# Kernel optimization log

Measured on AMD Instinct MI355X. Metric: run time of the kernel, lower is better.

The kernel has to match this reference:

```python
import jax, jax.numpy as jnp
import numpy as np

N_NODES = 100000
N_EDGES = 3200000
F_DIM = 128
UNITS = 128
K_HOPS = 3


def setup_inputs() -> dict:
    key = jax.random.key(0)
    k1, k2, k3, k4, k5 = jax.random.split(key, 5)
    edge_rows = jax.random.randint(k1, (N_EDGES,), 0, N_NODES, dtype=jnp.int32)
    edge_cols = jax.random.randint(k2, (N_EDGES,), 0, N_NODES, dtype=jnp.int32)
    # positive edge weights (e.g. normalized adjacency values)
    edge_vals = jax.random.uniform(k3, (N_EDGES,), dtype=jnp.float32) / 32.0
    x = jax.random.normal(k4, (N_NODES, F_DIM), dtype=jnp.float32)
    H = jax.random.normal(k5, (K_HOPS, F_DIM, UNITS), dtype=jnp.float32) * 0.05
    return {"edge_rows": edge_rows, "edge_cols": edge_cols,
            "edge_vals": edge_vals, "x": x, "H": H}


def reference(edge_rows, edge_cols, edge_vals, x, H):
    # spmm(h) = A @ h, with A given as an edge list (rows, cols, vals).
    def spmm(h):
        # gather source features, scale by edge weight, scatter-add to dest rows
        return jax.ops.segment_sum(edge_vals[:, None] * h[edge_cols],
                                   edge_rows, num_segments=N_NODES)

    # output = sum_{k=0}^{K-1} S_k @ (X @ H_k), S_0 = I, S_k = A^k
    out = x @ H[0]  # k = 0: identity propagation
    for k in range(1, K_HOPS):
        t = x @ H[k]           # [N, units] skinny GEMM
        for _ in range(k):     # apply A k times -> A^k @ t
            t = spmm(t)
        out = out + t
    return out  # activation is identity in defaults
```

## Files before the change

kernel.cpp:

```cpp
#include <hip/hip_runtime.h>

#define NN 100000
#define NE 3200000
#define FD 128
#define NBUK 782
#define NSEG (NBUK * 8)
#define NBIN 1024
#define CHUNK (NE / NBIN)
#define MAXB 5120

typedef __attribute__((ext_vector_type(8))) short short8;
typedef __attribute__((ext_vector_type(4))) float f32x4;

__device__ inline unsigned int f2bf_bits(float x) {
    unsigned int u = __float_as_uint(x);
    return (u + 0x7fffu + ((u >> 16) & 1u)) >> 16;
}
__device__ inline float bf_lo(unsigned int u) { return __uint_as_float(u << 16); }
__device__ inline float bf_hi(unsigned int u) { return __uint_as_float(u & 0xffff0000u); }

__global__ __launch_bounds__(256)
void cvt_x(const float* __restrict__ X, unsigned short* __restrict__ Xbf) {
    const int total = NN * FD / 4;
    const int stride = gridDim.x * blockDim.x;
    for (int i = blockIdx.x * blockDim.x + threadIdx.x; i < total; i += stride) {
        float4 v = reinterpret_cast<const float4*>(X)[i];
        uint2 o = make_uint2(f2bf_bits(v.x) | (f2bf_bits(v.y) << 16),
                             f2bf_bits(v.z) | (f2bf_bits(v.w) << 16));
        reinterpret_cast<uint2*>(Xbf)[i] = o;
    }
}

__global__ __launch_bounds__(256)
void cvt_h(const float* __restrict__ H, unsigned short* __restrict__ HbfT) {
    int i = blockIdx.x * 256 + threadIdx.x;
    if (i < 3 * FD * FD) {
        int k   = i >> 14;
        int rem = i & 16383;
        int kk  = rem >> 7;
        int col = rem & 127;
        HbfT[k * (FD * FD) + col * FD + kk] = (unsigned short)f2bf_bits(H[i]);
    }
}

__global__ __launch_bounds__(256, 4)
void gemm3_mfma(const unsigned short* __restrict__ Xbf,
                const unsigned short* __restrict__ HbfT,
                float* __restrict__ OUT,
                unsigned short* __restrict__ Vbf,
                unsigned short* __restrict__ T2bf) {
    __shared__ __align__(16) unsigned short Xs[128 * 128];
    const int tid  = threadIdx.x;
    const int row0 = blockIdx.x * 128;

    #pragma unroll
    for (int it = 0; it < 8; ++it) {
        int c    = it * 256 + tid;
        int r    = c >> 4;
        int col8 = (c & 15) * 8;
        int gr   = row0 + r;
        uint4 v = make_uint4(0u, 0u, 0u, 0u);
        if (gr < NN)
            v = *reinterpret_cast<const uint4*>(Xbf + (size_t)gr * FD + col8);
        int byte = r * 256 + col8 * 2;
        byte ^= (r & 7) << 4;
        *reinterpret_cast<uint4*>(reinterpret_cast<char*>(Xs) + byte) = v;
    }
    __syncthreads();

    const int lane = tid & 63;
    const int w    = tid >> 6;
    const int l15  = lane & 15;
    const int g4   = lane >> 4;

    int abyte[2];
    #pragma unroll
    for (int m = 0; m < 2; ++m) {
        int arow = 32 * w + 16 * m + l15;
        abyte[m] = arow * 256 + g4 * 16;
    }
    const int swz0 = (l15 & 7) << 4;

    #pragma unroll
    for (int h = 0; h < 3; ++h) {
        f32x4 acc[2][8];
        #pragma unroll
        for (int m = 0; m < 2; ++m)
            #pragma unroll
            for (int n = 0; n < 8; ++n) acc[m][n] = (f32x4)(0.f);

        const unsigned short* Hb = HbfT + h * (FD * FD) + l15 * FD + g4 * 8;

        #pragma unroll
        for (int ks = 0; ks < 4; ++ks) {
            short8 a0 = *reinterpret_cast<const short8*>(
                reinterpret_cast<const char*>(Xs) + ((abyte[0] + ks * 64) ^ swz0));
            short8 a1 = *reinterpret_cast<const short8*>(
                reinterpret_cast<const char*>(Xs) + ((abyte[1] + ks * 64) ^ swz0));
            #pragma unroll
            for (int n = 0; n < 8; ++n) {
                short8 b = *reinterpret_cast<const short8*>(Hb + n * (16 * FD) + ks * 32);
                acc[0][n] = __builtin_amdgcn_mfma_f32_16x16x32_bf16(a0, b, acc[0][n], 0, 0, 0);
                acc[1][n] = __builtin_amdgcn_mfma_f32_16x16x32_bf16(a1, b, acc[1][n], 0, 0, 0);
            }
        }

        #pragma unroll
        for (int m = 0; m < 2; ++m) {
            #pragma unroll
            for (int r = 0; r < 4; ++r) {
                int gr = row0 + 32 * w + 16 * m + g4 * 4 + r;
                if (gr < NN) {
                    if (h == 0) {
                        float* dst = OUT + (size_t)gr * FD + l15;
                        #pragma unroll
                        for (int n = 0; n < 8; ++n) dst[16 * n] = acc[m][n][r];
                    } else {
                        unsigned short* dst = (h == 1 ? Vbf : T2bf) + (size_t)gr * FD + l15;
                        #pragma unroll
                        for (int n = 0; n < 8; ++n)
                            dst[16 * n] = (unsigned short)f2bf_bits(acc[m][n][r]);
                    }
                }
            }
        }
    }
}

__global__ __launch_bounds__(256)
void zero_counts(int* __restrict__ counts) {
    int i = blockIdx.x * 256 + threadIdx.x;
    if (i < NSEG) counts[i] = 0;
}

__global__ __launch_bounds__(256)
void bucket_hist(const int* __restrict__ rows, int* __restrict__ counts) {
    __shared__ int lh[NBUK];
    for (int i = threadIdx.x; i < NBUK; i += 256) lh[i] = 0;
    __syncthreads();
    const int beg = blockIdx.x * CHUNK, end = beg + CHUNK;
    for (int e = beg + threadIdx.x; e < end; e += 256)
        atomicAdd(&lh[rows[e] >> 7], 1);
    __syncthreads();
    const int g = blockIdx.x & 7;
    for (int b = threadIdx.x; b < NBUK; b += 256)
        if (lh[b]) atomicAdd(&counts[b * 8 + g], lh[b]);
}

__global__ __launch_bounds__(1024)
void scan_segs(const int* __restrict__ counts, int* __restrict__ cursor,
               int* __restrict__ bucket_ptr) {
    __shared__ int s[1024];
    const int tid = threadIdx.x;
    const int per = (NSEG + 1023) / 1024;
    const int base = tid * per;
    int sum = 0;
    for (int i = 0; i < per; ++i) {
        int idx = base + i;
        if (idx < NSEG) sum += counts[idx];
    }
    s[tid] = sum;
    __syncthreads();
    for (int off = 1; off < 1024; off <<= 1) {
        int t = (tid >= off) ? s[tid - off] : 0;
        __syncthreads();
        s[tid] += t;
        __syncthreads();
    }
    int run = s[tid] - sum;
    for (int i = 0; i < per; ++i) {
        int idx = base + i;
        if (idx < NSEG) {
            cursor[idx] = run;
            if ((idx & 7) == 0) bucket_ptr[idx >> 3] = run;
            run += counts[idx];
        }
    }
    if (tid == 1023) bucket_ptr[NBUK] = NE;
}

__global__ __launch_bounds__(256)
void bin_scatter(const int* __restrict__ rows, const int* __restrict__ cols,
                 const float* __restrict__ vals, int* __restrict__ cursor,
                 uint2* __restrict__ recs) {
    const int beg = blockIdx.x * CHUNK, end = beg + CHUNK;
    const int g = blockIdx.x & 7;
    for (int e = beg + threadIdx.x; e < end; e += 256) {
        int r = rows[e];
        int b = r >> 7;
        int pos = atomicAdd(&cursor[b * 8 + g], 1);
        recs[pos] = make_uint2(((unsigned)(r & 127) << 17) | (unsigned)cols[e],
                               __float_as_uint(vals[e]));
    }
}

__global__ __launch_bounds__(256)
void bucket_csr(uint2* __restrict__ recs, const int* __restrict__ bucket_ptr,
                int* __restrict__ row_ptr) {
    __shared__ uint2 stage[MAXB];
    __shared__ int lh[128];
    __shared__ int lsc[128];
    const int b = blockIdx.x, tid = threadIdx.x;
    const int beg = bucket_ptr[b], end = bucket_ptr[b + 1];
    const int n = end - beg;

    if (tid < 128) lh[tid] = 0;
    __syncthreads();
    for (int i = tid; i < n; i += 256) {
        uint2 r = recs[beg + i];
        stage[i] = r;
        atomicAdd(&lh[r.x >> 17], 1);
    }
    __syncthreads();
    int v = (tid < 128) ? lh[tid] : 0;
    if (tid < 128) lsc[tid] = v;
    __syncthreads();
    for (int off = 1; off < 128; off <<= 1) {
        int t = 0;
        if (tid < 128 && tid >= off) t = lsc[tid - off];
        __syncthreads();
        if (tid < 128) lsc[tid] += t;
        __syncthreads();
    }
    if (tid < 128) {
        int excl = lsc[tid] - v;
        int gr = b * 128 + tid;
        if (gr <= NN) row_ptr[gr] = beg + excl;
        lh[tid] = excl;
    }
    __syncthreads();
    for (int i = tid; i < n; i += 256) {
        uint2 r = stage[i];
        int pos = atomicAdd(&lh[r.x >> 17], 1);
        recs[beg + pos] = r;
    }
}

#define SPMM_BODY(STORE)                                                       \
    const int lane = threadIdx.x & 63;                                         \
    const int row  = (blockIdx.x * blockDim.x + threadIdx.x) >> 6;             \
    if (row >= NN) return;                                                     \
    const int sub = lane >> 5;                     \
    const int fq  = lane & 31;                 \
    const int beg = row_ptr[row], end = row_ptr[row + 1];                      \
    float4 acc = make_float4(0.f, 0.f, 0.f, 0.f);                              \
    int e = beg + sub;                                                         \
    for (; e + 14 < end; e += 16) {                                            \
        uint2 p[8];                                                            \
        uint2 g[8];                                                            \
        _Pragma("unroll")                                                      \
        for (int u = 0; u < 8; ++u) p[u] = recs[e + 2 * u];                    \
        _Pragma("unroll")                                                      \
        for (int u = 0; u < 8; ++u)                                            \
            g[u] = *reinterpret_cast<const uint2*>(                            \
                src + (size_t)(p[u].x & 0x1FFFF) * FD + fq * 4);               \
        _Pragma("unroll")                                                      \
        for (int u = 0; u < 8; ++u) {                                          \
            float v = __uint_as_float(p[u].y);                                 \
            acc.x += v * bf_lo(g[u].x); acc.y += v * bf_hi(g[u].x);            \
            acc.z += v * bf_lo(g[u].y); acc.w += v * bf_hi(g[u].y);            \
        }                                                                      \
    }                                                                          \
    for (; e < end; e += 2) {                                                  \
        uint2 p = recs[e];                                                     \
        uint2 g = *reinterpret_cast<const uint2*>(                             \
            src + (size_t)(p.x & 0x1FFFF) * FD + fq * 4);                      \
        float v = __uint_as_float(p.y);                                        \
        acc.x += v * bf_lo(g.x); acc.y += v * bf_hi(g.x);                      \
        acc.z += v * bf_lo(g.y); acc.w += v * bf_hi(g.y);                      \
    }                                                                          \
    acc.x += __shfl_xor(acc.x, 32, 64);                                        \
    acc.y += __shfl_xor(acc.y, 32, 64);                                        \
    acc.z += __shfl_xor(acc.z, 32, 64);                                        \
    acc.w += __shfl_xor(acc.w, 32, 64);                                        \
    if (sub == 0) { STORE }

__global__ __launch_bounds__(256)
void spmm_bf_bf(const int* __restrict__ row_ptr, const uint2* __restrict__ recs,
                const unsigned short* __restrict__ src,
                unsigned short* __restrict__ initdst) {
    SPMM_BODY({
        uint2 iv = *reinterpret_cast<const uint2*>(initdst + (size_t)row * FD + fq * 4);
        acc.x += bf_lo(iv.x); acc.y += bf_hi(iv.x);
        acc.z += bf_lo(iv.y); acc.w += bf_hi(iv.y);
        unsigned int w0 = f2bf_bits(acc.x) | (f2bf_bits(acc.y) << 16);
        unsigned int w1 = f2bf_bits(acc.z) | (f2bf_bits(acc.w) << 16);
        *reinterpret_cast<uint2*>(initdst + (size_t)row * FD + fq * 4) = make_uint2(w0, w1);
    })
}

__global__ __launch_bounds__(256)
void spmm_bf_f32(const int* __restrict__ row_ptr, const uint2* __restrict__ recs,
                 const unsigned short* __restrict__ src, float* __restrict__ dst) {
    SPMM_BODY({
        float4 iv = *reinterpret_cast<const float4*>(dst + (size_t)row * FD + fq * 4);
        acc.x += iv.x; acc.y += iv.y; acc.z += iv.z; acc.w += iv.w;
        *reinterpret_cast<float4*>(dst + (size_t)row * FD + fq * 4) = acc;
    })
}

extern "C" void kernel_launch(void* const* d_in, const int* in_sizes, int n_in,
                              void* d_out, int out_size, void* d_ws, size_t ws_size,
                              hipStream_t stream) {
    const int*   edge_rows = (const int*)d_in[0];
    const int*   edge_cols = (const int*)d_in[1];
    const float* edge_vals = (const float*)d_in[2];
    const float* x         = (const float*)d_in[3];
    const float* H         = (const float*)d_in[4];
    float*       out       = (float*)d_out;

    const size_t feat = (size_t)NN * FD;
    unsigned short* Xbf  = (unsigned short*)d_ws;
    unsigned short* T2bf = Xbf + feat;
    unsigned short* Vbf  = T2bf + feat;
    unsigned short* HbfT = Vbf + feat;
    uint2*          recs = (uint2*)(HbfT + 3 * FD * FD);
    int* counts     = (int*)(recs + NE);
    int* cursor     = counts + NSEG;
    int* row_ptr    = cursor + NSEG;
    int* bucket_ptr = row_ptr + NN + 1;

    cvt_x<<<2048, 256, 0, stream>>>(x, Xbf);
    cvt_h<<<(3 * FD * FD + 255) / 256, 256, 0, stream>>>(H, HbfT);

    gemm3_mfma<<<(NN + 127) / 128, 256, 0, stream>>>(Xbf, HbfT, out, Vbf, T2bf);

    zero_counts<<<(NSEG + 255) / 256, 256, 0, stream>>>(counts);
    bucket_hist<<<NBIN, 256, 0, stream>>>(edge_rows, counts);
    scan_segs<<<1, 1024, 0, stream>>>(counts, cursor, bucket_ptr);
    bin_scatter<<<NBIN, 256, 0, stream>>>(edge_rows, edge_cols, edge_vals,
                                          cursor, recs);
    bucket_csr<<<NBUK, 256, 0, stream>>>(recs, bucket_ptr, row_ptr);

    const int spmm_blocks = (NN * 64 + 255) / 256;
    spmm_bf_bf <<<spmm_blocks, 256, 0, stream>>>(row_ptr, recs, T2bf, Vbf);
    spmm_bf_f32<<<spmm_blocks, 256, 0, stream>>>(row_ptr, recs, Vbf, out);
}
```

Measured before the change: 651.5 us.

## Fuse X bf16 conversion into GEMM and restructure CSR build into partition sort

The GEMM now reads fp32 X and converts to bf16 while staging into LDS, removing the separate cvt_x pass and its round-trip buffer. The CSR construction switches from 782 buckets of 128 rows with 8 sub-segments to 391 partitions of 256 rows. Per-block local histograms reserve contiguous ranges with one global atomic per partition, so the per-edge global atomics become LDS atomics. A row_sort pass then writes into a second record buffer instead of staging in shared memory. This adds an extra 25.6 MB workspace buffer and re-reads rows in the scatter kernel in exchange for fewer global atomics.

```diff
diff --git a/kernel.cpp b/kernel.cpp
--- a/kernel.cpp
+++ b/kernel.cpp
@@ -3,11 +3,10 @@
 #define NN 100000
 #define NE 3200000
 #define FD 128
-#define NBUK 782
-#define NSEG (NBUK * 8)
-#define NBIN 1024
-#define CHUNK (NE / NBIN)
-#define MAXB 5120
+#define PROWS 256
+#define NPART 391
+#define PBIN 512
+#define PCHUNK (NE / PBIN)
 
 typedef __attribute__((ext_vector_type(8))) short short8;
 typedef __attribute__((ext_vector_type(4))) float f32x4;
@@ -18,18 +17,6 @@
 }
 __device__ inline float bf_lo(unsigned int u) { return __uint_as_float(u << 16); }
 __device__ inline float bf_hi(unsigned int u) { return __uint_as_float(u & 0xffff0000u); }
-
-__global__ __launch_bounds__(256)
-void cvt_x(const float* __restrict__ X, unsigned short* __restrict__ Xbf) {
-    const int total = NN * FD / 4;
-    const int stride = gridDim.x * blockDim.x;
-    for (int i = blockIdx.x * blockDim.x + threadIdx.x; i < total; i += stride) {
-        float4 v = reinterpret_cast<const float4*>(X)[i];
-        uint2 o = make_uint2(f2bf_bits(v.x) | (f2bf_bits(v.y) << 16),
-                             f2bf_bits(v.z) | (f2bf_bits(v.w) << 16));
-        reinterpret_cast<uint2*>(Xbf)[i] = o;
-    }
-}
 
 __global__ __launch_bounds__(256)
 void cvt_h(const float* __restrict__ H, unsigned short* __restrict__ HbfT) {
@@ -44,7 +31,7 @@
 }
 
 __global__ __launch_bounds__(256, 4)
-void gemm3_mfma(const unsigned short* __restrict__ Xbf,
+void gemm3_mfma(const float* __restrict__ X,
                 const unsigned short* __restrict__ HbfT,
                 float* __restrict__ OUT,
                 unsigned short* __restrict__ Vbf,
@@ -60,8 +47,14 @@
         int col8 = (c & 15) * 8;
         int gr   = row0 + r;
         uint4 v = make_uint4(0u, 0u, 0u, 0u);
-        if (gr < NN)
-            v = *reinterpret_cast<const uint4*>(Xbf + (size_t)gr * FD + col8);
+        if (gr < NN) {
+            float4 a = *reinterpret_cast<const float4*>(X + (size_t)gr * FD + col8);
+            float4 b = *reinterpret_cast<const float4*>(X + (size_t)gr * FD + col8 + 4);
+            v.x = f2bf_bits(a.x) | (f2bf_bits(a.y) << 16);
+            v.y = f2bf_bits(a.z) | (f2bf_bits(a.w) << 16);
+            v.z = f2bf_bits(b.x) | (f2bf_bits(b.y) << 16);
+            v.w = f2bf_bits(b.z) | (f2bf_bits(b.w) << 16);
+        }
         int byte = r * 256 + col8 * 2;
         byte ^= (r & 7) << 4;
         *reinterpret_cast<uint4*>(reinterpret_cast<char*>(Xs) + byte) = v;
@@ -127,112 +120,100 @@
     }
 }
 
-__global__ __launch_bounds__(256)
-void zero_counts(int* __restrict__ counts) {
-    int i = blockIdx.x * 256 + threadIdx.x;
-    if (i < NSEG) counts[i] = 0;
-}
-
-__global__ __launch_bounds__(256)
-void bucket_hist(const int* __restrict__ rows, int* __restrict__ counts) {
-    __shared__ int lh[NBUK];
-    for (int i = threadIdx.x; i < NBUK; i += 256) lh[i] = 0;
-    __syncthreads();
-    const int beg = blockIdx.x * CHUNK, end = beg + CHUNK;
+__global__ __launch_bounds__(512)
+void zero_small(int* __restrict__ p, int n) {
+    int i = blockIdx.x * 512 + threadIdx.x;
+    if (i < n) p[i] = 0;
+}
+
+__global__ __launch_bounds__(256)
+void phist(const int* __restrict__ rows, int* __restrict__ pcount) {
+    __shared__ int lh[NPART];
+    for (int i = threadIdx.x; i < NPART; i += 256) lh[i] = 0;
+    __syncthreads();
+    const int beg = blockIdx.x * PCHUNK, end = beg + PCHUNK;
     for (int e = beg + threadIdx.x; e < end; e += 256)
-        atomicAdd(&lh[rows[e] >> 7], 1);
-    __syncthreads();
-    const int g = blockIdx.x & 7;
-    for (int b = threadIdx.x; b < NBUK; b += 256)
-        if (lh[b]) atomicAdd(&counts[b * 8 + g], lh[b]);
-}
-
-__global__ __launch_bounds__(1024)
-void scan_segs(const int* __restrict__ counts, int* __restrict__ cursor,
-               int* __restrict__ bucket_ptr) {
-    __shared__ int s[1024];
+        atomicAdd(&lh[rows[e] >> 8], 1);
+    __syncthreads();
+    for (int i = threadIdx.x; i < NPART; i += 256)
+        if (lh[i]) atomicAdd(&pcount[i], lh[i]);
+}
+
+__global__ __launch_bounds__(512)
+void pscan(const int* __restrict__ pcount, int* __restrict__ pbase,
+           int* __restrict__ pcursor) {
+    __shared__ int s[512];
     const int tid = threadIdx.x;
-    const int per = (NSEG + 1023) / 1024;
-    const int base = tid * per;
-    int sum = 0;
-    for (int i = 0; i < per; ++i) {
-        int idx = base + i;
-        if (idx < NSEG) sum += counts[idx];
-    }
-    s[tid] = sum;
-    __syncthreads();
-    for (int off = 1; off < 1024; off <<= 1) {
+    int v = (tid < NPART) ? pcount[tid] : 0;
+    s[tid] = v;
+    __syncthreads();
+    for (int off = 1; off < 512; off <<= 1) {
         int t = (tid >= off) ? s[tid - off] : 0;
         __syncthreads();
         s[tid] += t;
         __syncthreads();
     }
-    int run = s[tid] - sum;
-    for (int i = 0; i < per; ++i) {
-        int idx = base + i;
-        if (idx < NSEG) {
-            cursor[idx] = run;
-            if ((idx & 7) == 0) bucket_ptr[idx >> 3] = run;
-            run += counts[idx];
-        }
-    }
-    if (tid == 1023) bucket_ptr[NBUK] = NE;
-}
-
-__global__ __launch_bounds__(256)
-void bin_scatter(const int* __restrict__ rows, const int* __restrict__ cols,
-                 const float* __restrict__ vals, int* __restrict__ cursor,
-                 uint2* __restrict__ recs) {
-    const int beg = blockIdx.x * CHUNK, end = beg + CHUNK;
-    const int g = blockIdx.x & 7;
+    int excl = s[tid] - v;
+    if (tid < NPART) { pbase[tid] = excl; pcursor[tid] = excl; }
+    if (tid == 0) pbase[NPART] = NE;
+}
+
+__global__ __launch_bounds__(256)
+void part_scatter(const int* __restrict__ rows, const int* __restrict__ cols,
+                  const float* __restrict__ vals, int* __restrict__ pcursor,
+                  uint2* __restrict__ recs) {
+    __shared__ int lh[NPART];
+    __shared__ int lcur[NPART];
+    for (int i = threadIdx.x; i < NPART; i += 256) lh[i] = 0;
+    __syncthreads();
+    const int beg = blockIdx.x * PCHUNK, end = beg + PCHUNK;
+    for (int e = beg + threadIdx.x; e < end; e += 256)
+        atomicAdd(&lh[rows[e] >> 8], 1);
+    __syncthreads();
+    for (int i = threadIdx.x; i < NPART; i += 256)
+        lcur[i] = lh[i] ? atomicAdd(&pcursor[i], lh[i]) : 0;
+    __syncthreads();
     for (int e = beg + threadIdx.x; e < end; e += 256) {
         int r = rows[e];
-        int b = r >> 7;
-        int pos = atomicAdd(&cursor[b * 8 + g], 1);
-        recs[pos] = make_uint2(((unsigned)(r & 127) << 17) | (unsigned)cols[e],
+        int p = r >> 8;
+        int pos = atomicAdd(&lcur[p], 1);
+        recs[pos] = make_uint2(((unsigned)(r & 255) << 17) | (unsigned)cols[e],
                                __float_as_uint(vals[e]));
     }
 }
 
 __global__ __launch_bounds__(256)
-void bucket_csr(uint2* __restrict__ recs, const int* __restrict__ bucket_ptr,
-                int* __restrict__ row_ptr) {
-    __shared__ uint2 stage[MAXB];
-    __shared__ int lh[128];
-    __shared__ int lsc[128];
-    const int b = blockIdx.x, tid = threadIdx.x;
-    const int beg = bucket_ptr[b], end = bucket_ptr[b + 1];
-    const int n = end - beg;
-
-    if (tid < 128) lh[tid] = 0;
-    __syncthreads();
-    for (int i = tid; i < n; i += 256) {
-        uint2 r = recs[beg + i];
-        stage[i] = r;
-        atomicAdd(&lh[r.x >> 17], 1);
-    }
-    __syncthreads();
-    int v = (tid < 128) ? lh[tid] : 0;
-    if (tid < 128) lsc[tid] = v;
-    __syncthreads();
-    for (int off = 1; off < 128; off <<= 1) {
-        int t = 0;
-        if (tid < 128 && tid >= off) t = lsc[tid - off];
+void row_sort(const uint2* __restrict__ recs, const int* __restrict__ pbase,
+              uint2* __restrict__ recs2, int* __restrict__ row_ptr) {
+    __shared__ int rh[256];
+    __shared__ int rsc[256];
+    __shared__ int rcur[256];
+    const int p = blockIdx.x, tid = threadIdx.x;
+    const int beg = pbase[p], end = pbase[p + 1];
+
+    rh[tid] = 0;
+    __syncthreads();
+    for (int i = beg + tid; i < end; i += 256)
+        atomicAdd(&rh[recs[i].x >> 17], 1);
+    __syncthreads();
+    int v = rh[tid];
+    rsc[tid] = v;
+    __syncthreads();
+    for (int off = 1; off < 256; off <<= 1) {
+        int t = (tid >= off) ? rsc[tid - off] : 0;
         __syncthreads();
-        if (tid < 128) lsc[tid] += t;
+        rsc[tid] += t;
         __syncthreads();
     }
-    if (tid < 128) {
-        int excl = lsc[tid] - v;
-        int gr = b * 128 + tid;
-        if (gr <= NN) row_ptr[gr] = beg + excl;
-        lh[tid] = excl;
-    }
-    __syncthreads();
-    for (int i = tid; i < n; i += 256) {
-        uint2 r = stage[i];
-        int pos = atomicAdd(&lh[r.x >> 17], 1);
-        recs[beg + pos] = r;
+    int excl = rsc[tid] - v;
+    int gr = p * PROWS + tid;
+    if (gr <= NN) row_ptr[gr] = beg + excl;
+    rcur[tid] = beg + excl;
+    __syncthreads();
+    for (int i = beg + tid; i < end; i += 256) {
+        uint2 u = recs[i];
+        int pos = atomicAdd(&rcur[u.x >> 17], 1);
+        recs2[pos] = u;
     }
 }
 
@@ -310,29 +291,27 @@
     float*       out       = (float*)d_out;
 
     const size_t feat = (size_t)NN * FD;
-    unsigned short* Xbf  = (unsigned short*)d_ws;
-    unsigned short* T2bf = Xbf + feat;
+    unsigned short* T2bf = (unsigned short*)d_ws;
     unsigned short* Vbf  = T2bf + feat;
     unsigned short* HbfT = Vbf + feat;
     uint2*          recs = (uint2*)(HbfT + 3 * FD * FD);
-    int* counts     = (int*)(recs + NE);
-    int* cursor     = counts + NSEG;
-    int* row_ptr    = cursor + NSEG;
-    int* bucket_ptr = row_ptr + NN + 1;
-
-    cvt_x<<<2048, 256, 0, stream>>>(x, Xbf);
+    uint2*          recs2 = recs + NE;
+    int* pcount  = (int*)(recs2 + NE);
+    int* pbase   = pcount + NPART;
+    int* pcursor = pbase + NPART + 1;
+    int* row_ptr = pcursor + NPART;
+
     cvt_h<<<(3 * FD * FD + 255) / 256, 256, 0, stream>>>(H, HbfT);
-
-    gemm3_mfma<<<(NN + 127) / 128, 256, 0, stream>>>(Xbf, HbfT, out, Vbf, T2bf);
-
-    zero_counts<<<(NSEG + 255) / 256, 256, 0, stream>>>(counts);
-    bucket_hist<<<NBIN, 256, 0, stream>>>(edge_rows, counts);
-    scan_segs<<<1, 1024, 0, stream>>>(counts, cursor, bucket_ptr);
-    bin_scatter<<<NBIN, 256, 0, stream>>>(edge_rows, edge_cols, edge_vals,
-                                          cursor, recs);
-    bucket_csr<<<NBUK, 256, 0, stream>>>(recs, bucket_ptr, row_ptr);
+    gemm3_mfma<<<(NN + 127) / 128, 256, 0, stream>>>(x, HbfT, out, Vbf, T2bf);
+
+    zero_small<<<1, 512, 0, stream>>>(pcount, NPART);
+    phist<<<PBIN, 256, 0, stream>>>(edge_rows, pcount);
+    pscan<<<1, 512, 0, stream>>>(pcount, pbase, pcursor);
+    part_scatter<<<PBIN, 256, 0, stream>>>(edge_rows, edge_cols, edge_vals,
+                                           pcursor, recs);
+    row_sort<<<NPART, 256, 0, stream>>>(recs, pbase, recs2, row_ptr);
 
     const int spmm_blocks = (NN * 64 + 255) / 256;
-    spmm_bf_bf <<<spmm_blocks, 256, 0, stream>>>(row_ptr, recs, T2bf, Vbf);
-    spmm_bf_f32<<<spmm_blocks, 256, 0, stream>>>(row_ptr, recs, Vbf, out);
-}
+    spmm_bf_bf <<<spmm_blocks, 256, 0, stream>>>(row_ptr, recs2, T2bf, Vbf);
+    spmm_bf_f32<<<spmm_blocks, 256, 0, stream>>>(row_ptr, recs2, Vbf, out);
+}
```

Measured after the change: 555.5 us. 14.7% less time.
